# Performance work log

Measured on AMD Instinct MI355X. Metric: run time of the kernel, lower is better.

The kernel has to match this reference:

```python
import jax, jax.numpy as jnp
import numpy as np

COS_EPS = 1e-8  # torch.nn.CosineSimilarity default eps
B, L, D = 32, 512, 1024
S, E = 256, 64
POS = 17


def _padded_idxs(key, batch, max_len, seq_len, min_frac=0.5):
    """Random first-subword indices in [1, seq_len) with trailing zero padding."""
    k1, k2 = jax.random.split(key)
    lens = jax.random.randint(k1, (batch,), int(max_len * min_frac), max_len + 1)
    vals = jax.random.randint(k2, (batch, max_len), 1, seq_len)
    col = jnp.arange(max_len)[None, :]
    return jnp.where(col < lens[:, None], vals, 0).astype(jnp.int32)


def setup_inputs() -> dict:
    key = jax.random.key(0)
    ks = jax.random.split(key, 7)
    all_embeddings = jax.random.normal(ks[0], (B, L, D), dtype=jnp.float32)
    W = jax.random.uniform(ks[1], (D, D), dtype=jnp.float32) / np.sqrt(D)
    lin_w = jax.random.normal(ks[2], (2, 2 * D + POS), dtype=jnp.float32) * 0.02
    lin_b = jnp.zeros((2,), dtype=jnp.float32)
    idxs_to_collect_sent = _padded_idxs(ks[3], B, S, L)
    idxs_to_collect_event = _padded_idxs(ks[4], B, E, L)
    pos_tag = jax.random.randint(ks[5], (B, S), -1, POS - 1).astype(jnp.int32)
    return {
        "all_embeddings": all_embeddings,
        "W": W,
        "lin_w": lin_w,
        "lin_b": lin_b,
        "idxs_to_collect_sent": idxs_to_collect_sent,
        "idxs_to_collect_event": idxs_to_collect_event,
        "pos_tag": pos_tag,
    }


def _gather_pad(all_embeddings, idxs):
    # idxs has valid (>0) entries at the front, zeros as trailing pad, so the
    # per-sample compact-gather-then-pad loop is equivalent to gather + mask.
    mask = (idxs > 0)  # [B, T]
    gathered = jnp.take_along_axis(
        all_embeddings, jnp.maximum(idxs, 0)[..., None], axis=1)  # [B, T, D]
    return gathered * mask[..., None].astype(all_embeddings.dtype), mask


def reference(all_embeddings, W, lin_w, lin_b,
              idxs_to_collect_sent, idxs_to_collect_event, pos_tag):
    sent, _ = _gather_pad(all_embeddings, idxs_to_collect_sent)       # [B,S,D]
    event, ev_mask = _gather_pad(all_embeddings, idxs_to_collect_event)  # [B,E,D]

    # map_numerator = 1 / number of valid event tokens per sample
    map_num = 1.0 / jnp.sum(ev_mask, axis=-1).astype(sent.dtype)  # [B]

    # cosine similarity between (sent @ W) and event embeddings
    a = jnp.einsum('bsd,de->bse', sent, W)                 # [B,S,D]
    num = jnp.einsum('bsd,bed->bse', a, event)             # [B,S,E]
    na = jnp.maximum(jnp.linalg.norm(a, axis=-1), COS_EPS)       # [B,S]
    ne = jnp.maximum(jnp.linalg.norm(event, axis=-1), COS_EPS)   # [B,E]
    logits = num / (na[:, :, None] * ne[:, None, :])       # [B,S,E]

    sent2event_att = jnp.einsum('bse,bed->bsd', logits, event) * map_num[:, None, None]

    pos = jnp.where(pos_tag < 0, POS - 1, pos_tag)
    pos_oh = jax.nn.one_hot(pos, POS, dtype=sent.dtype)    # [B,S,17]

    feat = jnp.concatenate([sent, sent2event_att, pos_oh], axis=-1)  # [B,S,2D+17]
    return feat @ lin_w.T + lin_b                           # [B,S,2]
```

## Files before the change

kernel.cpp:

```cpp
#include <hip/hip_runtime.h>

#define B_ 32
#define L_ 512
#define D_ 1024
#define S_ 256
#define E_ 64
#define POS_ 17
#define LWS 2065
#define M_ (B_*S_)

typedef __attribute__((ext_vector_type(8))) short short8v;
typedef __attribute__((ext_vector_type(4))) float f32x4;
typedef __attribute__((ext_vector_type(16))) float f32x16;
typedef __attribute__((ext_vector_type(4))) unsigned short us4;

__device__ __forceinline__ unsigned short f2bf(float x) {
  union { float f; unsigned u; } v; v.f = x;
  unsigned r = v.u + 0x7FFFu + ((v.u >> 16) & 1u);
  return (unsigned short)(r >> 16);
}
__device__ __forceinline__ float bf2f(unsigned short b) {
  union { unsigned u; float f; } v; v.u = ((unsigned)b) << 16;
  return v.f;
}
__device__ __forceinline__ void async16(void* lds, const void* g) {
  __builtin_amdgcn_global_load_lds(
      (const __attribute__((address_space(1))) unsigned int*)(unsigned long long)g,
      (__attribute__((address_space(3))) unsigned int*)(unsigned int)(unsigned long long)lds,
      16, 0, 0);
}

#define VMCNT8 asm volatile("s_waitcnt vmcnt(8)" ::: "memory")
#define VMCNT0 asm volatile("s_waitcnt vmcnt(0)" ::: "memory")
#define BARRIER __builtin_amdgcn_s_barrier()

__global__ __launch_bounds__(256) void prep_all(
    const float* __restrict__ emb, const float* __restrict__ W,
    const float* __restrict__ lin_w, const float* __restrict__ lin_b,
    const int* __restrict__ idx_s, const int* __restrict__ idx_e,
    const int* __restrict__ pos_tag,
    unsigned short* __restrict__ sentb, unsigned short* __restrict__ evb,
    unsigned short* __restrict__ Wt,
    float* __restrict__ base, float* __restrict__ ne, float* __restrict__ evw) {
  __shared__ float tile[32][33];
  __shared__ float red[12];
  int bid = blockIdx.x;
  int t = threadIdx.x;
  int lane = t & 63, w = t >> 6;

  if (bid >= 10240) {
    int tt = bid - 10240;
    int bx = tt & 31, by = tt >> 5;
    int tx = t & 31, ty = t >> 5;
#pragma unroll
    for (int i = 0; i < 4; i++)
      tile[ty + i * 8][tx] = W[(size_t)(by * 32 + ty + i * 8) * D_ + bx * 32 + tx];
    __syncthreads();
#pragma unroll
    for (int i = 0; i < 4; i++)
      Wt[(size_t)(bx * 32 + ty + i * 8) * D_ + by * 32 + tx] = f2bf(tile[tx][ty + i * 8]);
    return;
  }

  bool is_sent = bid < M_;
  int row = is_sent ? bid : bid - M_;
  int b = is_sent ? (row >> 8) : (row >> 6);
  int idx = is_sent ? idx_s[row] : idx_e[row];
  float msk = idx > 0 ? 1.0f : 0.0f;
  const float* src = emb + ((size_t)b * L_ + (idx > 0 ? idx : 0)) * D_;
  float4 v = *(const float4*)(src + t * 4);
  v.x *= msk; v.y *= msk; v.z *= msk; v.w *= msk;
  us4 o; o.x = f2bf(v.x); o.y = f2bf(v.y); o.z = f2bf(v.z); o.w = f2bf(v.w);
  int d = t * 4;

  if (is_sent) {
    *(us4*)&sentb[(size_t)row * D_ + d] = o;
    const float* lw0 = lin_w;
    const float* lw1 = lin_w + LWS;
    float l0 = v.x * lw0[d] + v.y * lw0[d + 1] + v.z * lw0[d + 2] + v.w * lw0[d + 3];
    float l1 = v.x * lw1[d] + v.y * lw1[d + 1] + v.z * lw1[d + 2] + v.w * lw1[d + 3];
#pragma unroll
    for (int off = 32; off; off >>= 1) {
      l0 += __shfl_xor(l0, off);
      l1 += __shfl_xor(l1, off);
    }
    if (lane == 0) { red[w * 2] = l0; red[w * 2 + 1] = l1; }
    __syncthreads();
    if (t == 0) {
      float L0 = red[0] + red[2] + red[4] + red[6];
      float L1 = red[1] + red[3] + red[5] + red[7];
      int p = pos_tag[row]; if (p < 0) p = POS_ - 1;
      base[(size_t)row * 2 + 0] = L0 + lin_b[0] + lin_w[2 * D_ + p];
      base[(size_t)row * 2 + 1] = L1 + lin_b[1] + lin_w[LWS + 2 * D_ + p];
    }
  } else {
    *(us4*)&evb[(size_t)row * D_ + d] = o;
    const float* lw0 = lin_w + D_;
    const float* lw1 = lin_w + LWS + D_;
    float sq = v.x * v.x + v.y * v.y + v.z * v.z + v.w * v.w;
    float e0 = v.x * lw0[d] + v.y * lw0[d + 1] + v.z * lw0[d + 2] + v.w * lw0[d + 3];
    float e1 = v.x * lw1[d] + v.y * lw1[d + 1] + v.z * lw1[d + 2] + v.w * lw1[d + 3];
#pragma unroll
    for (int off = 32; off; off >>= 1) {
      sq += __shfl_xor(sq, off);
      e0 += __shfl_xor(e0, off);
      e1 += __shfl_xor(e1, off);
    }
    if (lane == 0) { red[w * 3] = sq; red[w * 3 + 1] = e0; red[w * 3 + 2] = e1; }
    __syncthreads();
    if (t == 0) {
      float SQ = red[0] + red[3] + red[6] + red[9];
      float E0 = red[1] + red[4] + red[7] + red[10];
      float E1 = red[2] + red[5] + red[8] + red[11];
      ne[row] = fmaxf(sqrtf(SQ), 1e-8f);
      evw[(size_t)row * 2 + 0] = E0;
      evw[(size_t)row * 2 + 1] = E1;
    }
  }
}

__device__ __forceinline__ void stage_g(const char* gA, const char* gB,
    unsigned short* bA, unsigned short* bB, int t, int kt) {
  int sc = ((t & 7) ^ ((t >> 3) & 7)) << 4;
#pragma unroll
  for (int i = 0; i < 4; i++) {
    int row = i * 32 + (t >> 3);
    size_t src = (size_t)row * (D_ * 2) + (size_t)kt * 128 + sc;
    async16((char*)bA + i * 4096 + t * 16, gA + src);
    async16((char*)bB + i * 4096 + t * 16, gB + src);
  }
}
__device__ __forceinline__ void comp_g(const unsigned short* bA,
    const unsigned short* bB, f32x16 (&acc)[2][2], int wr, int wc, int fr32, int hi1) {
  int x = fr32 & 7;
#pragma unroll
  for (int ks = 0; ks < 4; ks++) {
    int co = ((ks * 2 + hi1) ^ x) << 3;
    short8v a[2], bv[2];
#pragma unroll
    for (int m = 0; m < 2; m++)
      a[m] = *(const short8v*)&bA[(wr * 64 + m * 32 + fr32) * 64 + co];
#pragma unroll
    for (int n = 0; n < 2; n++)
      bv[n] = *(const short8v*)&bB[(wc * 64 + n * 32 + fr32) * 64 + co];
#pragma unroll
    for (int m = 0; m < 2; m++)
#pragma unroll
      for (int n = 0; n < 2; n++)
        acc[m][n] = __builtin_amdgcn_mfma_f32_32x32x16_bf16(a[m], bv[n], acc[m][n], 0, 0, 0);
  }
}

__global__ __launch_bounds__(256) void gemm_aw(
    const unsigned short* __restrict__ A,
    const unsigned short* __restrict__ Bt,
    unsigned short* __restrict__ C) {
  const int K = D_, N = D_;
  __shared__ unsigned short sA0[128 * 64], sA1[128 * 64];
  __shared__ unsigned short sB0[128 * 64], sB1[128 * 64];
  int t = threadIdx.x;
  int w = t >> 6, lane = t & 63;
  int wr = w >> 1, wc = w & 1;
  int fr32 = lane & 31, hi1 = lane >> 5;
  int bid = blockIdx.x;
  int wg = ((bid & 7) << 6) | (bid >> 3);
  int n0 = (wg & 7) * 128, m0 = (wg >> 3) * 128;
  f32x16 acc[2][2];
#pragma unroll
  for (int m = 0; m < 2; m++)
#pragma unroll
    for (int n = 0; n < 2; n++)
#pragma unroll
      for (int r = 0; r < 16; r++) acc[m][n][r] = 0.f;

  const char* gA = (const char*)(A + (size_t)m0 * K);
  const char* gB = (const char*)(Bt + (size_t)n0 * K);

  stage_g(gA, gB, sA0, sB0, t, 0);
#pragma unroll 1
  for (int kt = 0; kt < 14; kt += 2) {
    stage_g(gA, gB, sA1, sB1, t, kt + 1);
    VMCNT8; BARRIER;
    __builtin_amdgcn_sched_barrier(0);
    comp_g(sA0, sB0, acc, wr, wc, fr32, hi1);
    BARRIER;
    stage_g(gA, gB, sA0, sB0, t, kt + 2);
    VMCNT8; BARRIER;
    __builtin_amdgcn_sched_barrier(0);
    comp_g(sA1, sB1, acc, wr, wc, fr32, hi1);
    BARRIER;
  }
  stage_g(gA, gB, sA1, sB1, t, 15);
  VMCNT8; BARRIER;
  __builtin_amdgcn_sched_barrier(0);
  comp_g(sA0, sB0, acc, wr, wc, fr32, hi1);
  VMCNT0; BARRIER;
  __builtin_amdgcn_sched_barrier(0);
  comp_g(sA1, sB1, acc, wr, wc, fr32, hi1);

#pragma unroll
  for (int m = 0; m < 2; m++) {
#pragma unroll
    for (int n = 0; n < 2; n++) {
#pragma unroll
      for (int r = 0; r < 16; r++) {
        int crow = (r & 3) + 8 * (r >> 2) + 4 * hi1;
        int row = wr * 64 + m * 32 + crow;
        C[(size_t)(m0 + row) * N + n0 + wc * 64 + n * 32 + fr32] = f2bf(acc[m][n][r]);
      }
    }
  }
}

__device__ __forceinline__ void stage_a(const char* gA, const char* gE,
    unsigned short* bA, unsigned short* bE, int t, int kt) {
  int sc = ((t & 7) ^ ((t >> 3) & 7)) << 4;
  int row = t >> 3;
  async16((char*)bA + t * 16, gA + (size_t)row * (D_ * 2) + (size_t)kt * 128 + sc);
#pragma unroll
  for (int i = 0; i < 2; i++) {
    int er = i * 32 + row;
    async16((char*)bE + i * 4096 + t * 16, gE + (size_t)er * (D_ * 2) + (size_t)kt * 128 + sc);
  }
}
__device__ __forceinline__ void comp_a(const unsigned short* bA,
    const unsigned short* bE, f32x4 (&acc)[2], float& rsq, int w, int fr, int hi) {
  int x = fr & 7;
  int rowA = (w >> 1) * 16 + fr;
  int ch = w & 1;
#pragma unroll
  for (int ks = 0; ks < 2; ks++) {
    int co = ((ks * 4 + hi) ^ x) << 3;
    short8v af = *(const short8v*)&bA[rowA * 64 + co];
    if (ch == 0) {
#pragma unroll
      for (int j = 0; j < 8; j++) { float xv = bf2f((unsigned short)af[j]); rsq += xv * xv; }
    }
#pragma unroll
    for (int n = 0; n < 2; n++) {
      short8v bv = *(const short8v*)&bE[(ch * 32 + n * 16 + fr) * 64 + co];
      acc[n] = __builtin_amdgcn_mfma_f32_16x16x32_bf16(af, bv, acc[n], 0, 0, 0);
    }
  }
}

__global__ __launch_bounds__(256) void attn_ep(
    const unsigned short* __restrict__ Abf,
    const unsigned short* __restrict__ Ebf,
    const int* __restrict__ idx_e,
    const float* __restrict__ ne, const float* __restrict__ evw,
    const float* __restrict__ base,
    float* __restrict__ out) {
  int b = blockIdx.x >> 3;
  int s0 = (blockIdx.x & 7) * 32;
  __shared__ unsigned short sA0[32 * 64], sA1[32 * 64];
  __shared__ unsigned short sE0[64 * 64], sE1[64 * 64];
  __shared__ float sRne[E_], sEvw[E_][2], sRna[32], sP[2][32][2];
  __shared__ float sMapn;
  int t = threadIdx.x;
  int w = t >> 6, lane = t & 63;
  int fr = lane & 15, hi = lane >> 4;
  if (t < E_) {
    sRne[t] = 1.0f / ne[b * E_ + t];
    sEvw[t][0] = evw[(size_t)(b * E_ + t) * 2 + 0];
    sEvw[t][1] = evw[(size_t)(b * E_ + t) * 2 + 1];
    unsigned long long mball = __ballot(idx_e[b * E_ + t] > 0);
    if (t == 0) sMapn = 1.0f / (float)__popcll(mball);
  }
  f32x4 acc[2];
#pragma unroll
  for (int n = 0; n < 2; n++) acc[n] = f32x4{0.f, 0.f, 0.f, 0.f};
  float rsq = 0.f;

  const char* gA = (const char*)(Abf + ((size_t)b * S_ + s0) * D_);
  const char* gE = (const char*)(Ebf + (size_t)b * E_ * D_);

  stage_a(gA, gE, sA0, sE0, t, 0);
  __syncthreads();
#pragma unroll 1
  for (int kt = 0; kt < 16; kt += 2) {
    stage_a(gA, gE, sA1, sE1, t, kt + 1);
    comp_a(sA0, sE0, acc, rsq, w, fr, hi);
    __syncthreads();
    if (kt + 2 < 16) stage_a(gA, gE, sA0, sE0, t, kt + 2);
    comp_a(sA1, sE1, acc, rsq, w, fr, hi);
    __syncthreads();
  }
  rsq += __shfl_xor(rsq, 16);
  rsq += __shfl_xor(rsq, 32);
  if ((w & 1) == 0 && lane < 16)
    sRna[(w >> 1) * 16 + lane] = 1.0f / fmaxf(sqrtf(rsq), 1e-8f);
  __syncthreads();

  int ch = w & 1;
#pragma unroll
  for (int r = 0; r < 4; r++) {
    int srl = (w >> 1) * 16 + hi * 4 + r;
    float rna = sRna[srl];
    float a0 = 0.f, a1 = 0.f;
#pragma unroll
    for (int n = 0; n < 2; n++) {
      int e = ch * 32 + n * 16 + fr;
      float lg = acc[n][r] * rna * sRne[e];
      a0 += lg * sEvw[e][0];
      a1 += lg * sEvw[e][1];
    }
#pragma unroll
    for (int off = 1; off < 16; off <<= 1) {
      a0 += __shfl_xor(a0, off);
      a1 += __shfl_xor(a1, off);
    }
    if (fr == 0) { sP[ch][srl][0] = a0; sP[ch][srl][1] = a1; }
  }
  __syncthreads();
  if (t < 64) {
    int row = t >> 1, c = t & 1;
    float v = sP[0][row][c] + sP[1][row][c];
    size_t sg = (size_t)b * S_ + s0 + row;
    out[sg * 2 + c] = base[sg * 2 + c] + sMapn * v;
  }
}

extern "C" void kernel_launch(void* const* d_in, const int* in_sizes, int n_in,
                              void* d_out, int out_size, void* d_ws, size_t ws_size,
                              hipStream_t stream) {
  const float* emb   = (const float*)d_in[0];
  const float* W     = (const float*)d_in[1];
  const float* lin_w = (const float*)d_in[2];
  const float* lin_b = (const float*)d_in[3];
  const int* idx_s   = (const int*)d_in[4];
  const int* idx_e   = (const int*)d_in[5];
  const int* pos     = (const int*)d_in[6];
  float* out = (float*)d_out;

  char* ws = (char*)d_ws;
  const size_t MB = 1024 * 1024;
  unsigned short* sentb = (unsigned short*)(ws);
  unsigned short* abf   = (unsigned short*)(ws + 16 * MB);
  unsigned short* evb   = (unsigned short*)(ws + 32 * MB);
  unsigned short* Wt    = (unsigned short*)(ws + 36 * MB);
  float* ne   = (float*)(ws + 38 * MB);
  float* evw  = ne + 2048;
  float* base = evw + 4096;

  prep_all<<<M_ + B_ * E_ + 1024, 256, 0, stream>>>(
      emb, W, lin_w, lin_b, idx_s, idx_e, pos, sentb, evb, Wt, base, ne, evw);
  gemm_aw<<<512, 256, 0, stream>>>(sentb, Wt, abf);
  attn_ep<<<B_ * 8, 256, 0, stream>>>(abf, evb, idx_e, ne, evw, base, out);
}
```

Before: 47.66 us.

## Double attention K-tile to 128, swizzle per-row, and remap blocks across XCDs

The attention kernel now stages 128-wide K tiles instead of 64, with a 16-chunk XOR swizzle. This halves the number of loop iterations and barriers, at the cost of doubled shared memory per buffer. Block indices in both the gather and attention kernels are remapped so that blocks sharing a batch land on the same XCD, which is meant to improve L2 reuse of the event and sentence rows. The larger LDS footprint may reduce occupancy.

```diff
diff --git a/kernel.cpp b/kernel.cpp
--- a/kernel.cpp
+++ b/kernel.cpp
@@ -63,7 +63,7 @@
   }
 
   bool is_sent = bid < M_;
-  int row = is_sent ? bid : bid - M_;
+  int row = is_sent ? (((bid & 7) << 10) | (bid >> 3)) : (bid - M_);
   int b = is_sent ? (row >> 8) : (row >> 6);
   int idx = is_sent ? idx_s[row] : idx_e[row];
   float msk = idx > 0 ? 1.0f : 0.0f;
@@ -214,31 +214,38 @@
 
 __device__ __forceinline__ void stage_a(const char* gA, const char* gE,
     unsigned short* bA, unsigned short* bE, int t, int kt) {
-  int sc = ((t & 7) ^ ((t >> 3) & 7)) << 4;
-  int row = t >> 3;
-  async16((char*)bA + t * 16, gA + (size_t)row * (D_ * 2) + (size_t)kt * 128 + sc);
 #pragma unroll
   for (int i = 0; i < 2; i++) {
-    int er = i * 32 + row;
-    async16((char*)bE + i * 4096 + t * 16, gE + (size_t)er * (D_ * 2) + (size_t)kt * 128 + sc);
+    int idx = i * 256 + t;
+    int row = idx >> 4;
+    int ch = (idx & 15) ^ (row & 15);
+    async16((char*)bA + idx * 16, gA + (size_t)row * (D_ * 2) + (size_t)kt * 256 + ch * 16);
+  }
+#pragma unroll
+  for (int i = 0; i < 4; i++) {
+    int idx = i * 256 + t;
+    int row = idx >> 4;
+    int ch = (idx & 15) ^ (row & 15);
+    async16((char*)bE + idx * 16, gE + (size_t)row * (D_ * 2) + (size_t)kt * 256 + ch * 16);
   }
 }
 __device__ __forceinline__ void comp_a(const unsigned short* bA,
     const unsigned short* bE, f32x4 (&acc)[2], float& rsq, int w, int fr, int hi) {
-  int x = fr & 7;
   int rowA = (w >> 1) * 16 + fr;
   int ch = w & 1;
 #pragma unroll
-  for (int ks = 0; ks < 2; ks++) {
-    int co = ((ks * 4 + hi) ^ x) << 3;
-    short8v af = *(const short8v*)&bA[rowA * 64 + co];
+  for (int ks = 0; ks < 4; ks++) {
+    int ca = ((ks * 4 + hi) ^ (rowA & 15)) << 3;
+    short8v af = *(const short8v*)&bA[rowA * 128 + ca];
     if (ch == 0) {
 #pragma unroll
       for (int j = 0; j < 8; j++) { float xv = bf2f((unsigned short)af[j]); rsq += xv * xv; }
     }
 #pragma unroll
     for (int n = 0; n < 2; n++) {
-      short8v bv = *(const short8v*)&bE[(ch * 32 + n * 16 + fr) * 64 + co];
+      int rowE = ch * 32 + n * 16 + fr;
+      int ce = ((ks * 4 + hi) ^ (rowE & 15)) << 3;
+      short8v bv = *(const short8v*)&bE[rowE * 128 + ce];
       acc[n] = __builtin_amdgcn_mfma_f32_16x16x32_bf16(af, bv, acc[n], 0, 0, 0);
     }
   }
@@ -251,10 +258,12 @@
     const float* __restrict__ ne, const float* __restrict__ evw,
     const float* __restrict__ base,
     float* __restrict__ out) {
-  int b = blockIdx.x >> 3;
-  int s0 = (blockIdx.x & 7) * 32;
-  __shared__ unsigned short sA0[32 * 64], sA1[32 * 64];
-  __shared__ unsigned short sE0[64 * 64], sE1[64 * 64];
+  int bid = blockIdx.x;
+  int xcd = bid & 7, loc = bid >> 3;
+  int b = xcd * 4 + (loc >> 3);
+  int s0 = (loc & 7) * 32;
+  __shared__ unsigned short sA0[32 * 128], sA1[32 * 128];
+  __shared__ unsigned short sE0[64 * 128], sE1[64 * 128];
   __shared__ float sRne[E_], sEvw[E_][2], sRna[32], sP[2][32][2];
   __shared__ float sMapn;
   int t = threadIdx.x;
@@ -278,11 +287,11 @@
   stage_a(gA, gE, sA0, sE0, t, 0);
   __syncthreads();
 #pragma unroll 1
-  for (int kt = 0; kt < 16; kt += 2) {
+  for (int kt = 0; kt < 8; kt += 2) {
     stage_a(gA, gE, sA1, sE1, t, kt + 1);
     comp_a(sA0, sE0, acc, rsq, w, fr, hi);
     __syncthreads();
-    if (kt + 2 < 16) stage_a(gA, gE, sA0, sE0, t, kt + 2);
+    if (kt + 2 < 8) stage_a(gA, gE, sA0, sE0, t, kt + 2);
     comp_a(sA1, sE1, acc, rsq, w, fr, hi);
     __syncthreads();
   }
```

New measurement: 44.75 us. 1.06x faster.
